# Performance work log

Measured on AMD Instinct MI355X. Metric: run time of the kernel, lower is better.

## Reference

```python
import jax, jax.numpy as jnp
import numpy as np

BASE = 10000.0

def _rope(x):
    # x: [b, n, h, d]; positions along token axis n, rotate-half convention
    d = x.shape[-1]
    n = x.shape[1]
    inv_freq = 1.0 / (BASE ** (jnp.arange(0, d, 2, dtype=jnp.float32) / d))  # [d/2]
    t = jnp.arange(n, dtype=jnp.float32)
    freqs = jnp.outer(t, inv_freq)                       # [n, d/2]
    emb = jnp.concatenate([freqs, freqs], axis=-1)       # [n, d]
    cos = jnp.cos(emb)[None, :, None, :]
    sin = jnp.sin(emb)[None, :, None, :]
    x1, x2 = jnp.split(x, 2, axis=-1)
    rot = jnp.concatenate([-x2, x1], axis=-1)
    return x * cos + rot * sin


def setup_inputs() -> dict:
    key = jax.random.key(0)
    k1, k2, k3 = jax.random.split(key, 3)
    b, c, hh, ww = 64, 1024, 16, 16
    x = jax.random.normal(k1, (b, c, hh, ww), dtype=jnp.float32)
    w_qkv = jax.random.normal(k2, (3 * c, c), dtype=jnp.float32) * 0.02
    w_lin = jax.random.normal(k3, (c, c, 1, 1), dtype=jnp.float32) * 0.02
    b_lin = jnp.zeros((c,), dtype=jnp.float32)
    return {"x": x, "w_qkv": w_qkv, "w_lin": w_lin, "b_lin": b_lin, "n_heads": 16}


def reference(x, w_qkv, w_lin, b_lin, n_heads):
    b, c, hh, ww = x.shape
    n = hh * ww
    d_head = c // n_heads
    scale = d_head ** -0.5
    # flatten(2).transpose(-2,-1): [b, n, c]
    xt = jnp.transpose(x.reshape(b, c, n), (0, 2, 1))
    # qkv proj, unflatten to [b, n, heads, 3*d_head], chunk along last dim
    qkv = (xt @ w_qkv.T).reshape(b, n, n_heads, 3 * d_head)
    q, k, v = jnp.split(qkv, 3, axis=-1)                  # each [b, n, h, d]
    q = _rope(q)
    k = _rope(k)
    q = jax.nn.softmax(q, axis=-1) * scale                # softmax over d_head
    k = jax.nn.softmax(k, axis=-2)                        # softmax over heads axis (as in torch code)
    # k^T @ v over the heads axis -> per-token [d_head, d_head] context
    context = jnp.einsum('bnhd,bnhe->bnde', k, v)
    o = jnp.einsum('bnhd,bnde->bnhe', q, context)         # [b, n, h, d]
    # transpose(-2,-1).reshape(b, c, h, w)
    o = jnp.transpose(o, (0, 1, 3, 2)).reshape(b, c, hh, ww)
    # 1x1 conv
    return jnp.einsum('bchw,oc->bohw', o, w_lin[:, :, 0, 0]) + b_lin[None, :, None, None]
```

## Files before the change

### kernel.cpp

```cpp
#include <hip/hip_runtime.h>
#include <hip/hip_bf16.h>
#include <math.h>

typedef __hip_bfloat16 hbf16;
typedef __attribute__((ext_vector_type(8))) __bf16    bf16x8;
typedef __attribute__((ext_vector_type(4))) float     f32x4;
typedef __attribute__((ext_vector_type(4))) _Float16  f16x4;
typedef __attribute__((ext_vector_type(8))) unsigned short u16x8;

#define C_    1024
#define NTOK  256
#define NH    16
#define J3    3072

__device__ __forceinline__ unsigned short fbits(float v){
    return __builtin_bit_cast(unsigned short, __float2bfloat16(v));
}
__device__ __forceinline__ __bf16 to_bf(float v){
    return __builtin_bit_cast(__bf16, __float2bfloat16(v));
}

__device__ __forceinline__ void gload_lds16(const __bf16* g, __bf16* l) {
    __builtin_amdgcn_global_load_lds((const __attribute__((address_space(1))) void*)g,
                                     (__attribute__((address_space(3))) void*)l, 16, 0, 0);
}

__global__ __launch_bounds__(256) void cvt_w(const float* __restrict__ wq,
                                             __bf16* __restrict__ wqo,
                                             const float* __restrict__ wl,
                                             __bf16* __restrict__ wlo) {
    const float* in; __bf16* out; int i;
    if (blockIdx.x < 3072) { in = wq; out = wqo; i = blockIdx.x * 256 + threadIdx.x; }
    else                   { in = wl; out = wlo; i = (blockIdx.x - 3072) * 256 + threadIdx.x; }
    float4 v = ((const float4*)in)[i];
    ushort4 u;
    u.x = fbits(v.x); u.y = fbits(v.y); u.z = fbits(v.z); u.w = fbits(v.w);
    ((ushort4*)out)[i] = u;
}

__global__ __launch_bounds__(256) void xpose_x(const float* __restrict__ X,
                                               __bf16* __restrict__ Xt) {
    __shared__ float t[32][36];
    const int b = blockIdx.z, k0 = blockIdx.y * 32, s0 = blockIdx.x * 32;
    const int tid = threadIdx.x;
    {
        int kl = tid >> 3, s4 = (tid & 7) * 4;
        float4 v = *(const float4*)(X + ((size_t)b << 18) + (size_t)(k0 + kl) * 256 + s0 + s4);
        t[kl][s4] = v.x; t[kl][s4 + 1] = v.y; t[kl][s4 + 2] = v.z; t[kl][s4 + 3] = v.w;
    }
    __syncthreads();
    {
        int sl = tid >> 3, k4 = (tid & 7) * 4;
        ushort4 u;
        u.x = fbits(t[k4][sl]); u.y = fbits(t[k4 + 1][sl]);
        u.z = fbits(t[k4 + 2][sl]); u.w = fbits(t[k4 + 3][sl]);
        *(ushort4*)(Xt + (size_t)(b * 256 + s0 + sl) * 1024 + k0 + k4) = u;
    }
}

template <int EPI>
__global__ __launch_bounds__(256) void mfma_gemm(const __bf16* __restrict__ A,
                                                 const __bf16* __restrict__ B,
                                                 void* __restrict__ Cout,
                                                 const float* __restrict__ bias) {
    __shared__ union __align__(16) {
        struct { __bf16 A[128 * 64]; __bf16 B[128 * 64]; } kl;
        __bf16 stY[128][136];
    } sm;

    const int tid  = threadIdx.x;
    const int wave = tid >> 6, lane = tid & 63;
    const int wm = wave & 1, wn = wave >> 1;
    const int m0 = blockIdx.x * 128, n0 = blockIdx.y * 128;

    const int srow = lane >> 3;
    const int lchunk = (lane & 7) ^ srow;

    f32x4 acc[4][4] = {};

    for (int kk = 0; kk < 1024; kk += 64) {
        #pragma unroll
        for (int g4 = 0; g4 < 4; ++g4) {
            const int g = g4 * 4 + wave;
            const int row = g * 8 + srow;
            gload_lds16(A + (((size_t)(m0 + row)) << 10) + kk + lchunk * 8,
                        &sm.kl.A[g * 512]);
            gload_lds16(B + (((size_t)(n0 + row)) << 10) + kk + lchunk * 8,
                        &sm.kl.B[g * 512]);
        }
        __syncthreads();

        #pragma unroll
        for (int t = 0; t < 2; ++t) {
            const int chunk = t * 4 + (lane >> 4);
            bf16x8 af[4], bf[4];
            #pragma unroll
            for (int mi = 0; mi < 4; ++mi) {
                int row = wm * 64 + mi * 16 + (lane & 15);
                af[mi] = *(const bf16x8*)&sm.kl.A[row * 64 + ((chunk ^ (row & 7)) << 3)];
            }
            #pragma unroll
            for (int ni = 0; ni < 4; ++ni) {
                int row = wn * 64 + ni * 16 + (lane & 15);
                bf[ni] = *(const bf16x8*)&sm.kl.B[row * 64 + ((chunk ^ (row & 7)) << 3)];
            }
            #pragma unroll
            for (int mi = 0; mi < 4; ++mi)
                #pragma unroll
                for (int ni = 0; ni < 4; ++ni)
                    acc[mi][ni] = __builtin_amdgcn_mfma_f32_16x16x32_bf16(
                        af[mi], bf[ni], acc[mi][ni], 0, 0, 0);
        }
        __syncthreads();
    }

    const int cl = lane & 15, rq = lane >> 4;

    if (EPI == 0) {
        __syncthreads();
        #pragma unroll
        for (int mi = 0; mi < 4; ++mi)
            #pragma unroll
            for (int ni = 0; ni < 4; ++ni) {
                int row = wm * 64 + mi * 16 + rq * 4;
                int col = wn * 64 + ni * 16 + cl;
                #pragma unroll
                for (int j = 0; j < 4; ++j)
                    sm.stY[row + j][col] = to_bf(acc[mi][ni][j]);
            }
        __syncthreads();
        __bf16* Y = (__bf16*)Cout;
        #pragma unroll
        for (int i = 0; i < 8; ++i) {
            int cid = tid + 256 * i;
            int r = cid >> 4, c8 = (cid & 15) * 8;
            *(bf16x8*)(Y + (size_t)(m0 + r) * 3072 + n0 + c8) =
                *(const bf16x8*)&sm.stY[r][c8];
        }
    } else {
        float* out = (float*)Cout;
        float bia[4][4];
        const int rbase = m0 + wm * 64 + rq * 4;
        #pragma unroll
        for (int mi = 0; mi < 4; ++mi)
            #pragma unroll
            for (int j = 0; j < 4; ++j) bia[mi][j] = bias[rbase + mi * 16 + j];
        const int nbase = n0 + wn * 64 + cl;
        #pragma unroll
        for (int mi = 0; mi < 4; ++mi)
            #pragma unroll
            for (int ni = 0; ni < 4; ++ni) {
                int nn = nbase + ni * 16;
                size_t base = ((size_t)(nn >> 8) << 18) + (nn & 255);
                #pragma unroll
                for (int j = 0; j < 4; ++j) {
                    int oc = rbase + mi * 16 + j;
                    out[base + ((size_t)oc << 8)] = acc[mi][ni][j] + bia[mi][j];
                }
            }
    }
}

__global__ __launch_bounds__(1024) void attn_mfma(const __bf16* __restrict__ Y,
                                                  __bf16* __restrict__ Ot) {
    __shared__ union __align__(16) {
        __bf16  v[16][1024];
        ushort4 ost[256][16];
    } sm;

    const int tid  = threadIdx.x;
    const int wave = tid >> 6, lane = tid & 63;
    const int bb = blockIdx.x >> 4;
    const int n0 = (blockIdx.x & 15) * 16;
    const int n  = n0 + wave;
    const int quad = lane >> 4, m = lane & 15;
    const __bf16* Yt = Y + (size_t)(bb * 256 + n) * J3;

    #pragma unroll
    for (int p = 0; p < 2; ++p) {
        const int h = p * 8 + (lane >> 3), part = lane & 7;
        gload_lds16(Yt + h * 192 + 128 + part * 8, &sm.v[wave][p * 512]);
    }

    bf16x8 qb[2], kb[2];
    #pragma unroll
    for (int st = 0; st < 2; ++st) {
        qb[st] = *(const bf16x8*)(Yt + m * 192 +      st * 32 + quad * 8);
        kb[st] = *(const bf16x8*)(Yt + m * 192 + 64 + st * 32 + quad * 8);
    }
    float qf[16], kf[16];
    #pragma unroll
    for (int st = 0; st < 2; ++st)
        #pragma unroll
        for (int j = 0; j < 8; ++j) {
            qf[st * 8 + j] = (float)qb[st][j];
            kf[st * 8 + j] = (float)kb[st][j];
        }

    const float fn = (float)n;
    #pragma unroll
    for (int j = 0; j < 8; ++j) {
        const float d  = (float)(quad * 8 + j);
        const float th = fn * __expf(-0.28782313662425572f * d);
        const float sn = __sinf(th), cn = __cosf(th);
        float a0 = qf[j], a1 = qf[8 + j];
        qf[j]     = a0 * cn - a1 * sn;
        qf[8 + j] = a1 * cn + a0 * sn;
        float b0 = kf[j], b1 = kf[8 + j];
        kf[j]     = b0 * cn - b1 * sn;
        kf[8 + j] = b1 * cn + b0 * sn;
    }

    float qe[16], ls = 0.f;
    #pragma unroll
    for (int i = 0; i < 16; ++i) { qe[i] = __expf(qf[i]); ls += qe[i]; }
    ls += __shfl_xor(ls, 16);
    ls += __shfl_xor(ls, 32);
    const float qinv = 0.125f * __builtin_amdgcn_rcpf(ls);
    bf16x8 qbh[2];
    #pragma unroll
    for (int st = 0; st < 2; ++st)
        #pragma unroll
        for (int j = 0; j < 8; ++j) qbh[st][j] = to_bf(qe[st * 8 + j] * qinv);

    float ke[16], kc[16];
    #pragma unroll
    for (int i = 0; i < 16; ++i) { ke[i] = __expf(kf[i]); kc[i] = ke[i]; }
    #pragma unroll
    for (int msk = 1; msk <= 8; msk <<= 1)
        #pragma unroll
        for (int i = 0; i < 16; ++i) kc[i] += __shfl_xor(kc[i], msk);
    bf16x8 kbh[2];
    #pragma unroll
    for (int st = 0; st < 2; ++st)
        #pragma unroll
        for (int j = 0; j < 8; ++j)
            kbh[st][j] = to_bf(ke[st * 8 + j] * __builtin_amdgcn_rcpf(kc[st * 8 + j]));

    f32x4 Sp = {0.f, 0.f, 0.f, 0.f};
    Sp = __builtin_amdgcn_mfma_f32_16x16x32_bf16(kbh[0], qbh[0], Sp, 0, 0, 0);
    Sp = __builtin_amdgcn_mfma_f32_16x16x32_bf16(kbh[1], qbh[1], Sp, 0, 0, 0);

    __syncthreads();

    f32x4 o4[4];
#if __has_builtin(__builtin_amdgcn_mfma_f32_16x16x16f16)
    f16x4 af;
    #pragma unroll
    for (int r = 0; r < 4; ++r) af[r] = (_Float16)Sp[r];
    #pragma unroll
    for (int tile = 0; tile < 4; ++tile) {
        f16x4 bv;
        #pragma unroll
        for (int j = 0; j < 4; ++j)
            bv[j] = (_Float16)(float)sm.v[wave][(quad * 4 + j) * 64 + tile * 16 + m];
        f32x4 z = {0.f, 0.f, 0.f, 0.f};
        o4[tile] = __builtin_amdgcn_mfma_f32_16x16x16f16(af, bv, z, 0, 0, 0);
    }
#else
    bf16x8 a2;
    #pragma unroll
    for (int j = 0; j < 8; ++j) {
        int k = quad * 8 + j;
        int src = ((k & 15) >> 2) * 16 + m;
        float v = __shfl(Sp[k & 3], src, 64);
        a2[j] = (quad < 2) ? to_bf(v) : to_bf(0.f);
    }
    #pragma unroll
    for (int tile = 0; tile < 4; ++tile) {
        bf16x8 bv;
        #pragma unroll
        for (int j = 0; j < 8; ++j) {
            int k = quad * 8 + j;
            int kk = (k < 16) ? k : 0;
            bv[j] = sm.v[wave][kk * 64 + tile * 16 + m];
        }
        f32x4 z = {0.f, 0.f, 0.f, 0.f};
        o4[tile] = __builtin_amdgcn_mfma_f32_16x16x32_bf16(a2, bv, z, 0, 0, 0);
    }
#endif

    __syncthreads();

    #pragma unroll
    for (int r = 0; r < 4; ++r) {
        const int s = m * 16 + quad * 4 + r;
        const int phys = wave ^ (quad * 4 + r) ^ m;
        ushort4 u;
        u.x = fbits(o4[0][r]); u.y = fbits(o4[1][r]);
        u.z = fbits(o4[2][r]); u.w = fbits(o4[3][r]);
        sm.ost[s][phys] = u;
    }
    __syncthreads();

    {
        const int row = tid >> 2;
        const int w0  = (tid & 3) * 4;
        ushort4 u4[4];
        #pragma unroll
        for (int j = 0; j < 4; ++j) {
            const int phys = (w0 + j) ^ (row & 15) ^ (row >> 4);
            u4[j] = sm.ost[row][phys];
        }
        __bf16* dst = Ot + (((size_t)(bb * 256 + row)) << 10) + n0 * 4 + w0 * 4;
        u16x8 a = {u4[0].x, u4[0].y, u4[0].z, u4[0].w, u4[1].x, u4[1].y, u4[1].z, u4[1].w};
        u16x8 b = {u4[2].x, u4[2].y, u4[2].z, u4[2].w, u4[3].x, u4[3].y, u4[3].z, u4[3].w};
        *(u16x8*)dst = a;
        *(u16x8*)(dst + 8) = b;
    }
}

extern "C" void kernel_launch(void* const* d_in, const int* in_sizes, int n_in,
                              void* d_out, int out_size, void* d_ws, size_t ws_size,
                              hipStream_t stream) {
    const float* x     = (const float*)d_in[0];
    const float* w_qkv = (const float*)d_in[1];
    const float* w_lin = (const float*)d_in[2];
    const float* b_lin = (const float*)d_in[3];
    float* out = (float*)d_out;

    char* ws = (char*)d_ws;
    __bf16* Y    = (__bf16*)ws;
    __bf16* XtOt = (__bf16*)(ws + (size_t)100663296);
    __bf16* Wqb  = (__bf16*)(ws + (size_t)134217728);
    __bf16* Wlb  = (__bf16*)(ws + (size_t)140509184);

    cvt_w<<<4096, 256, 0, stream>>>(w_qkv, Wqb, w_lin, Wlb);
    xpose_x<<<dim3(8, 32, 64), 256, 0, stream>>>(x, XtOt);

    mfma_gemm<0><<<dim3(128, 24), 256, 0, stream>>>(XtOt, Wqb, (void*)Y, nullptr);
    attn_mfma<<<1024, 1024, 0, stream>>>(Y, XtOt);
    mfma_gemm<1><<<dim3(8, 128), 256, 0, stream>>>(Wlb, XtOt, (void*)out, b_lin);
}
```

Before: 342.5 us.

## Replace QKV projection GEMM with 256x256-tile triple-buffered MFMA kernel

Adds a new GEMM kernel for the QKV projection that uses 256x256 output tiles with 512 threads and a three-stage LDS ring filled through direct global-to-LDS loads, waited on with explicit vmcnt counts. Blocks are remapped in groups so neighbouring workgroups share A tiles for L2 reuse, and wave priority is raised around the MFMA bursts. The goal is higher arithmetic intensity and better overlap of loads with compute than the previous 128x128 kernel. The cost is more accumulator registers and LDS per block, which lowers occupancy, and the ring logic depends on hand-tuned wait counts.

```diff
diff --git a/kernel.cpp b/kernel.cpp
--- a/kernel.cpp
+++ b/kernel.cpp
@@ -58,6 +58,114 @@
     }
 }
 
+#define WAITVM(N) asm volatile("s_waitcnt vmcnt(" #N ")" ::: "memory")
+
+__device__ __forceinline__ void stage_tile(const __bf16* __restrict__ Ag,
+                                           const __bf16* __restrict__ Bg,
+                                           __bf16* sa, __bf16* sb,
+                                           int kk, int wave, int lane) {
+    const int rl = lane >> 2;
+    const int cg = (lane & 3) ^ ((lane >> 3) & 3);
+    const int coff = kk + cg * 8;
+    #pragma unroll
+    for (int i = 0; i < 2; ++i) {
+        const int seg = wave * 2 + i;
+        const int row = seg * 16 + rl;
+        gload_lds16(Ag + ((size_t)row << 10) + coff, sa + seg * 512);
+        gload_lds16(Bg + ((size_t)row << 10) + coff, sb + seg * 512);
+    }
+}
+
+__global__ __launch_bounds__(512, 2) void gemm256(const __bf16* __restrict__ A,
+                                                  const __bf16* __restrict__ B,
+                                                  __bf16* __restrict__ Y) {
+    __shared__ union __align__(16) {
+        struct { __bf16 A[3 * 8192]; __bf16 B[3 * 8192]; } kl;
+        __bf16 st[128][264];
+    } sm;
+
+    const int tid  = threadIdx.x;
+    const int wave = tid >> 6, lane = tid & 63;
+    const int wm = wave >> 2, wn = wave & 3;
+    const int quad = lane >> 4, m = lane & 15;
+
+    const int wg = blockIdx.x;
+    const int local = wg >> 3;
+    const int mb = (wg & 7) * 8 + (local & 7);
+    const int nb = local >> 3;
+    const int m0 = mb << 8, n0 = nb << 8;
+
+    const __bf16* Ab = A + ((size_t)m0 << 10);
+    const __bf16* Bb = B + ((size_t)n0 << 10);
+
+    const int pcs  = quad ^ ((lane >> 1) & 3);
+    const int aoff = (wm * 128 + m) * 32 + pcs * 8;
+    const int boff = (wn * 64  + m) * 32 + pcs * 8;
+
+    f32x4 acc[8][4] = {};
+
+    stage_tile(Ab, Bb, sm.kl.A,         sm.kl.B,         0,  wave, lane);
+    stage_tile(Ab, Bb, sm.kl.A + 8192,  sm.kl.B + 8192,  32, wave, lane);
+
+    int bt = 0, b2 = 2;
+    for (int t = 0; t < 32; ++t) {
+        if (t < 31) { WAITVM(4); } else { WAITVM(0); }
+        __builtin_amdgcn_sched_barrier(0);
+        __builtin_amdgcn_s_barrier();
+        __builtin_amdgcn_sched_barrier(0);
+
+        if (t < 30)
+            stage_tile(Ab, Bb, sm.kl.A + b2 * 8192, sm.kl.B + b2 * 8192,
+                       (t + 2) << 5, wave, lane);
+
+        const __bf16* sa = sm.kl.A + bt * 8192 + aoff;
+        const __bf16* sb = sm.kl.B + bt * 8192 + boff;
+        bf16x8 bfr[4], afr[8];
+        #pragma unroll
+        for (int ni = 0; ni < 4; ++ni) bfr[ni] = *(const bf16x8*)(sb + ni * 512);
+        #pragma unroll
+        for (int mi = 0; mi < 8; ++mi) afr[mi] = *(const bf16x8*)(sa + mi * 512);
+
+        __builtin_amdgcn_s_setprio(1);
+        #pragma unroll
+        for (int mi = 0; mi < 8; ++mi)
+            #pragma unroll
+            for (int ni = 0; ni < 4; ++ni)
+                acc[mi][ni] = __builtin_amdgcn_mfma_f32_16x16x32_bf16(
+                    afr[mi], bfr[ni], acc[mi][ni], 0, 0, 0);
+        __builtin_amdgcn_s_setprio(0);
+
+        bt = (bt == 2) ? 0 : bt + 1;
+        b2 = (b2 == 2) ? 0 : b2 + 1;
+    }
+
+    __syncthreads();
+    #pragma unroll
+    for (int h = 0; h < 2; ++h) {
+        if (wm == h) {
+            #pragma unroll
+            for (int mi = 0; mi < 8; ++mi)
+                #pragma unroll
+                for (int ni = 0; ni < 4; ++ni) {
+                    const int r = mi * 16 + quad * 4;
+                    const int c = wn * 64 + ni * 16 + m;
+                    #pragma unroll
+                    for (int j = 0; j < 4; ++j)
+                        sm.st[r + j][c] = to_bf(acc[mi][ni][j]);
+                }
+        }
+        __syncthreads();
+        #pragma unroll
+        for (int i = 0; i < 8; ++i) {
+            const int cid = i * 512 + tid;
+            const int r = cid >> 5, ch = (cid & 31) * 8;
+            *(bf16x8*)(Y + (size_t)(m0 + h * 128 + r) * 3072 + n0 + ch) =
+                *(const bf16x8*)&sm.st[r][ch];
+        }
+        __syncthreads();
+    }
+}
+
 template <int EPI>
 __global__ __launch_bounds__(256) void mfma_gemm(const __bf16* __restrict__ A,
                                                  const __bf16* __restrict__ B,
@@ -328,7 +436,7 @@
     cvt_w<<<4096, 256, 0, stream>>>(w_qkv, Wqb, w_lin, Wlb);
     xpose_x<<<dim3(8, 32, 64), 256, 0, stream>>>(x, XtOt);
 
-    mfma_gemm<0><<<dim3(128, 24), 256, 0, stream>>>(XtOt, Wqb, (void*)Y, nullptr);
+    gemm256<<<768, 512, 0, stream>>>(XtOt, Wqb, Y);
     attn_mfma<<<1024, 1024, 0, stream>>>(Y, XtOt);
     mfma_gemm<1><<<dim3(8, 128), 256, 0, stream>>>(Wlb, XtOt, (void*)out, b_lin);
 }
```

Result: faster. 323.7 us (-5.5%).

## Replace GEMM with 256x256-tile triple-buffered pipelined MFMA kernel

Applied to the files above, without the earlier changes.

Replaces the 128x128 single-buffered GEMM with a 512-thread 256x256-tile kernel. It uses K-step 32, a three-stage LDS ring filled by direct global-to-LDS loads, register double-buffered fragments and s_setprio around the MFMA bursts. A swizzled block-index mapping groups tiles for L2 reuse. The aim is to hide global-load latency behind MFMA and raise arithmetic intensity, at the cost of larger register and LDS use and fewer blocks per GEMM.

```diff
diff --git a/kernel.cpp b/kernel.cpp
--- a/kernel.cpp
+++ b/kernel.cpp
@@ -58,106 +58,166 @@
     }
 }
 
+#define WAITVM(N) asm volatile("s_waitcnt vmcnt(" #N ")" ::: "memory")
+
+__device__ __forceinline__ void stage_tile(const __bf16* __restrict__ Ag,
+                                           const __bf16* __restrict__ Bg,
+                                           __bf16* sa, __bf16* sb,
+                                           int kk, int wave, int lane) {
+    const int rl = lane >> 2;
+    const int cg = (lane & 3) ^ ((lane >> 3) & 3);
+    const int coff = kk + cg * 8;
+    #pragma unroll
+    for (int i = 0; i < 2; ++i) {
+        const int seg = wave * 2 + i;
+        const int row = seg * 16 + rl;
+        gload_lds16(Ag + ((size_t)row << 10) + coff, sa + seg * 512);
+        gload_lds16(Bg + ((size_t)row << 10) + coff, sb + seg * 512);
+    }
+}
+
+#define GBODY(BT, NBUF, T, DOSTG, DOPF, CA, CB, NA, NB)                        \
+  {                                                                            \
+    asm volatile("s_waitcnt vmcnt(0)" ::: "memory");                           \
+    __builtin_amdgcn_s_barrier();                                              \
+    __builtin_amdgcn_sched_barrier(0);                                         \
+    if (DOSTG) stage_tile(Ab, Bb, sm.kl.A + (((BT) + 2) % 3) * 8192,           \
+                          sm.kl.B + (((BT) + 2) % 3) * 8192, ((T) + 2) << 5,   \
+                          wave, lane);                                         \
+    bf16x8 h1[4];                                                              \
+    {                                                                          \
+      const __bf16* sa_ = sm.kl.A + (BT) * 8192 + aoff;                        \
+      _Pragma("unroll") for (int mi = 0; mi < 4; ++mi)                         \
+          h1[mi] = *(const bf16x8*)(sa_ + (mi + 4) * 512);                     \
+    }                                                                          \
+    if (DOPF) {                                                                \
+      const __bf16* na_ = sm.kl.A + (NBUF) * 8192 + aoff;                      \
+      const __bf16* nb_ = sm.kl.B + (NBUF) * 8192 + boff;                      \
+      _Pragma("unroll") for (int i = 0; i < 4; ++i) {                          \
+        NA[i] = *(const bf16x8*)(na_ + i * 512);                               \
+        NB[i] = *(const bf16x8*)(nb_ + i * 512);                               \
+      }                                                                        \
+    }                                                                          \
+    __builtin_amdgcn_s_setprio(1);                                             \
+    _Pragma("unroll") for (int mi = 0; mi < 4; ++mi)                           \
+      _Pragma("unroll") for (int ni = 0; ni < 4; ++ni)                         \
+        acc[mi][ni] = __builtin_amdgcn_mfma_f32_16x16x32_bf16(                 \
+            CA[mi], CB[ni], acc[mi][ni], 0, 0, 0);                             \
+    _Pragma("unroll") for (int mi = 0; mi < 4; ++mi)                           \
+      _Pragma("unroll") for (int ni = 0; ni < 4; ++ni)                         \
+        acc[mi + 4][ni] = __builtin_amdgcn_mfma_f32_16x16x32_bf16(             \
+            h1[mi], CB[ni], acc[mi + 4][ni], 0, 0, 0);                         \
+    __builtin_amdgcn_s_setprio(0);                                             \
+  }
+
 template <int EPI>
-__global__ __launch_bounds__(256) void mfma_gemm(const __bf16* __restrict__ A,
-                                                 const __bf16* __restrict__ B,
-                                                 void* __restrict__ Cout,
-                                                 const float* __restrict__ bias) {
+__global__ __launch_bounds__(512, 2) void gemm256(const __bf16* __restrict__ A,
+                                                  const __bf16* __restrict__ B,
+                                                  void* __restrict__ Cout,
+                                                  const float* __restrict__ bias) {
     __shared__ union __align__(16) {
-        struct { __bf16 A[128 * 64]; __bf16 B[128 * 64]; } kl;
-        __bf16 stY[128][136];
+        struct { __bf16 A[3 * 8192]; __bf16 B[3 * 8192]; } kl;
+        __bf16 st[128][264];
     } sm;
 
     const int tid  = threadIdx.x;
     const int wave = tid >> 6, lane = tid & 63;
-    const int wm = wave & 1, wn = wave >> 1;
-    const int m0 = blockIdx.x * 128, n0 = blockIdx.y * 128;
-
-    const int srow = lane >> 3;
-    const int lchunk = (lane & 7) ^ srow;
-
-    f32x4 acc[4][4] = {};
-
-    for (int kk = 0; kk < 1024; kk += 64) {
-        #pragma unroll
-        for (int g4 = 0; g4 < 4; ++g4) {
-            const int g = g4 * 4 + wave;
-            const int row = g * 8 + srow;
-            gload_lds16(A + (((size_t)(m0 + row)) << 10) + kk + lchunk * 8,
-                        &sm.kl.A[g * 512]);
-            gload_lds16(B + (((size_t)(n0 + row)) << 10) + kk + lchunk * 8,
-                        &sm.kl.B[g * 512]);
-        }
+    const int wm = wave >> 2, wn = wave & 3;
+    const int quad = lane >> 4, m = lane & 15;
+
+    const int wg = blockIdx.x;
+    int mb, nb;
+    if (EPI == 0) {
+        const int local = wg >> 3;
+        mb = (wg & 7) * 8 + (local & 7);
+        nb = local >> 3;
+    } else {
+        const int local = wg >> 3;
+        mb = local & 3;
+        nb = (wg & 7) * 8 + (local >> 2);
+    }
+    const int m0 = mb << 8, n0 = nb << 8;
+
+    const __bf16* Ab = A + ((size_t)m0 << 10);
+    const __bf16* Bb = B + ((size_t)n0 << 10);
+
+    const int pcs  = quad ^ ((lane >> 1) & 3);
+    const int aoff = (wm * 128 + m) * 32 + pcs * 8;
+    const int boff = (wn * 64  + m) * 32 + pcs * 8;
+
+    f32x4 acc[8][4] = {};
+    bf16x8 p0a[4], p0b[4], p1a[4], p1b[4];
+
+    stage_tile(Ab, Bb, sm.kl.A,        sm.kl.B,        0,  wave, lane);
+    stage_tile(Ab, Bb, sm.kl.A + 8192, sm.kl.B + 8192, 32, wave, lane);
+    WAITVM(4);
+    __builtin_amdgcn_s_barrier();
+    __builtin_amdgcn_sched_barrier(0);
+    #pragma unroll
+    for (int i = 0; i < 4; ++i) {
+        p0a[i] = *(const bf16x8*)(sm.kl.A + aoff + i * 512);
+        p0b[i] = *(const bf16x8*)(sm.kl.B + boff + i * 512);
+    }
+
+    for (int tt = 0; tt < 30; tt += 6) {
+        GBODY(0, 1, tt + 0, 1, 1, p0a, p0b, p1a, p1b);
+        GBODY(1, 2, tt + 1, 1, 1, p1a, p1b, p0a, p0b);
+        GBODY(2, 0, tt + 2, 1, 1, p0a, p0b, p1a, p1b);
+        GBODY(0, 1, tt + 3, 1, 1, p1a, p1b, p0a, p0b);
+        GBODY(1, 2, tt + 4, 1, 1, p0a, p0b, p1a, p1b);
+        GBODY(2, 0, tt + 5, 1, 1, p1a, p1b, p0a, p0b);
+    }
+    GBODY(0, 1, 30, 0, 1, p0a, p0b, p1a, p1b);
+    GBODY(1, 0, 31, 0, 0, p1a, p1b, p0a, p0b);
+
+    if (EPI == 0) {
         __syncthreads();
-
-        #pragma unroll
-        for (int t = 0; t < 2; ++t) {
-            const int chunk = t * 4 + (lane >> 4);
-            bf16x8 af[4], bf[4];
+        __bf16* Y = (__bf16*)Cout;
+        #pragma unroll
+        for (int h = 0; h < 2; ++h) {
+            if (wm == h) {
+                #pragma unroll
+                for (int mi = 0; mi < 8; ++mi)
+                    #pragma unroll
+                    for (int ni = 0; ni < 4; ++ni) {
+                        const int r = mi * 16 + quad * 4;
+                        const int c = wn * 64 + ni * 16 + m;
+                        #pragma unroll
+                        for (int j = 0; j < 4; ++j)
+                            sm.st[r + j][c] = to_bf(acc[mi][ni][j]);
+                    }
+            }
+            __syncthreads();
             #pragma unroll
-            for (int mi = 0; mi < 4; ++mi) {
-                int row = wm * 64 + mi * 16 + (lane & 15);
-                af[mi] = *(const bf16x8*)&sm.kl.A[row * 64 + ((chunk ^ (row & 7)) << 3)];
+            for (int i = 0; i < 8; ++i) {
+                const int cid = i * 512 + tid;
+                const int r = cid >> 5, ch = (cid & 31) * 8;
+                *(bf16x8*)(Y + (size_t)(m0 + h * 128 + r) * 3072 + n0 + ch) =
+                    *(const bf16x8*)&sm.st[r][ch];
             }
+            __syncthreads();
+        }
+    } else {
+        float* outp = (float*)Cout;
+        const int cl = lane & 15, rq = lane >> 4;
+        const int rbase = m0 + wm * 128 + rq * 4;
+        const int nbase = n0 + wn * 64 + cl;
+        #pragma unroll
+        for (int mi = 0; mi < 8; ++mi) {
+            float bia[4];
+            #pragma unroll
+            for (int j = 0; j < 4; ++j) bia[j] = bias[rbase + mi * 16 + j];
             #pragma unroll
             for (int ni = 0; ni < 4; ++ni) {
-                int row = wn * 64 + ni * 16 + (lane & 15);
-                bf[ni] = *(const bf16x8*)&sm.kl.B[row * 64 + ((chunk ^ (row & 7)) << 3)];
-            }
-            #pragma unroll
-            for (int mi = 0; mi < 4; ++mi)
-                #pragma unroll
-                for (int ni = 0; ni < 4; ++ni)
-                    acc[mi][ni] = __builtin_amdgcn_mfma_f32_16x16x32_bf16(
-                        af[mi], bf[ni], acc[mi][ni], 0, 0, 0);
-        }
-        __syncthreads();
-    }
-
-    const int cl = lane & 15, rq = lane >> 4;
-
-    if (EPI == 0) {
-        __syncthreads();
-        #pragma unroll
-        for (int mi = 0; mi < 4; ++mi)
-            #pragma unroll
-            for (int ni = 0; ni < 4; ++ni) {
-                int row = wm * 64 + mi * 16 + rq * 4;
-                int col = wn * 64 + ni * 16 + cl;
-                #pragma unroll
-                for (int j = 0; j < 4; ++j)
-                    sm.stY[row + j][col] = to_bf(acc[mi][ni][j]);
-            }
-        __syncthreads();
-        __bf16* Y = (__bf16*)Cout;
-        #pragma unroll
-        for (int i = 0; i < 8; ++i) {
-            int cid = tid + 256 * i;
-            int r = cid >> 4, c8 = (cid & 15) * 8;
-            *(bf16x8*)(Y + (size_t)(m0 + r) * 3072 + n0 + c8) =
-                *(const bf16x8*)&sm.stY[r][c8];
-        }
-    } else {
-        float* out = (float*)Cout;
-        float bia[4][4];
-        const int rbase = m0 + wm * 64 + rq * 4;
-        #pragma unroll
-        for (int mi = 0; mi < 4; ++mi)
-            #pragma unroll
-            for (int j = 0; j < 4; ++j) bia[mi][j] = bias[rbase + mi * 16 + j];
-        const int nbase = n0 + wn * 64 + cl;
-        #pragma unroll
-        for (int mi = 0; mi < 4; ++mi)
-            #pragma unroll
-            for (int ni = 0; ni < 4; ++ni) {
-                int nn = nbase + ni * 16;
-                size_t base = ((size_t)(nn >> 8) << 18) + (nn & 255);
+                const int nn = nbase + ni * 16;
+                const size_t base = ((size_t)(nn >> 8) << 18) + (nn & 255);
                 #pragma unroll
                 for (int j = 0; j < 4; ++j) {
-                    int oc = rbase + mi * 16 + j;
-                    out[base + ((size_t)oc << 8)] = acc[mi][ni][j] + bia[mi][j];
+                    const int oc = rbase + mi * 16 + j;
+                    outp[base + ((size_t)oc << 8)] = acc[mi][ni][j] + bia[j];
                 }
             }
+        }
     }
 }
 
@@ -328,7 +388,7 @@
     cvt_w<<<4096, 256, 0, stream>>>(w_qkv, Wqb, w_lin, Wlb);
     xpose_x<<<dim3(8, 32, 64), 256, 0, stream>>>(x, XtOt);
 
-    mfma_gemm<0><<<dim3(128, 24), 256, 0, stream>>>(XtOt, Wqb, (void*)Y, nullptr);
+    gemm256<0><<<768, 512, 0, stream>>>(XtOt, Wqb, (void*)Y, nullptr);
     attn_mfma<<<1024, 1024, 0, stream>>>(Y, XtOt);
-    mfma_gemm<1><<<dim3(8, 128), 256, 0, stream>>>(Wlb, XtOt, (void*)out, b_lin);
-}
+    gemm256<1><<<256, 512, 0, stream>>>(Wlb, XtOt, (void*)out, b_lin);
+}
```

Result: faster. 311.6 us (-9.0%).
